# Kernel optimization log

Measured on AMD Instinct MI355X. Metric: run time of the kernel, lower is better.

## Reference

```python
import jax, jax.numpy as jnp
import numpy as np

DIM = 180
HEADS = 6
HEAD_DIM = DIM // HEADS  # 30
WS = 16                  # window size
PWS = WS // 2            # permuted window size (8)
N = WS * WS              # 256 tokens per window
M = PWS * PWS            # 64 pooled kv tokens per window
B = 4                    # batch (images)
NW = 256                 # windows per image
BW = B * NW              # total windows (b_)
SCALE = HEAD_DIM ** -0.5


def _aligned_rel_index():
    # replicates the buffer construction in __init__ (torch.meshgrid default = 'ij')
    coords = np.stack(np.meshgrid(np.arange(PWS), np.arange(PWS), indexing='ij'))
    cf = coords.reshape(2, -1)
    rel = (cf[:, :, None] - cf[:, None, :]).transpose(1, 2, 0).copy()
    rel[:, :, 0] += PWS - 1
    rel[:, :, 1] += PWS - 1
    rel[:, :, 0] *= 2 * PWS - 1
    idx = rel.sum(-1)  # (M, M)
    idx = idx.reshape(PWS, PWS, 1, 1, M)
    idx = np.tile(idx, (1, 1, 2, 2, 1)).transpose(0, 2, 1, 3, 4).reshape(4 * M, M)
    return idx  # (N, M)


def setup_inputs() -> dict:
    key = jax.random.key(0)
    ks = jax.random.split(key, 10)
    num_bias = (2 * PWS - 1) * (2 * PWS - 1)  # 225
    inp = {
        'x': jax.random.normal(ks[0], (BW, N, DIM), jnp.float32),
        'k_v': jax.random.normal(ks[1], (B, 256), jnp.float32),
        'mask': jnp.zeros((NW, N, M), jnp.float32),
        'W_kernel': jax.random.normal(ks[2], (DIM * 2, 256), jnp.float32) * 0.02,
        'W_q': jax.random.normal(ks[3], (DIM, DIM), jnp.float32) * 0.02,
        'b_q': jnp.zeros((DIM,), jnp.float32),
        'W_kv': jax.random.normal(ks[4], (DIM // 2, DIM), jnp.float32) * 0.02,
        'b_kv': jnp.zeros((DIM // 2,), jnp.float32),
        'bias_table': jax.random.normal(ks[5], (num_bias, HEADS), jnp.float32) * 0.02,
        'W_proj': jax.random.normal(ks[6], (DIM, DIM), jnp.float32) * 0.02,
        'b_proj': jnp.zeros((DIM,), jnp.float32),
        'rel_index': jnp.asarray(_aligned_rel_index(), jnp.int32),
        'b': B,
        'windows_size': WS,
    }
    return inp


def reference(x, k_v, mask, W_kernel, W_q, b_q, W_kv, b_kv, bias_table,
              W_proj, b_proj, rel_index, b, windows_size):
    b_, n, c = x.shape
    # FiLM-style modulation: per-image scale/shift broadcast over all windows/tokens
    kv_mod = (k_v @ W_kernel.T).reshape(-1, 1, 1, 1, c * 2)   # (b,1,1,1,2c)
    k_v1, k_v2 = jnp.split(kv_mod, 2, axis=4)
    xr = x.reshape(b, -1, windows_size, windows_size, c)
    x = (xr * k_v1 + k_v2).reshape(b_, n, c)

    # pooled kv: 2x2 spatial pool packed into channels, split into k and v
    kv = (x @ W_kv.T + b_kv)
    kv = kv.reshape(b_, PWS, 2, PWS, 2, 2, c // 4)
    kv = kv.transpose(0, 1, 3, 5, 2, 4, 6).reshape(b_, n // 4, 2, HEADS, c // HEADS)
    kv = kv.transpose(2, 0, 3, 1, 4)                          # (2, b_, h, n//4, d)
    k, v = kv[0], kv[1]

    q = (x @ W_q.T + b_q).reshape(b_, n, HEADS, HEAD_DIM).transpose(0, 2, 1, 3)
    q = q * SCALE                                             # (b_, h, n, d)

    attn = jnp.einsum('bhnd,bhmd->bhnm', q, k)                # (b_, h, n, n//4)

    # gathered relative position bias
    rpb = bias_table[rel_index.reshape(-1)].reshape(n, n // 4, HEADS)
    attn = attn + rpb.transpose(2, 0, 1)[None]

    nw = mask.shape[0]
    attn = attn.reshape(b_ // nw, nw, HEADS, n, n // 4) + mask[None, :, None]
    attn = attn.reshape(-1, HEADS, n, n // 4)
    attn = jax.nn.softmax(attn, axis=-1)

    out = jnp.einsum('bhnm,bhmd->bhnd', attn, v)
    out = out.transpose(0, 2, 1, 3).reshape(b_, n, c)
    return out @ W_proj.T + b_proj
```

## Files before the change

### kernel.cpp

```cpp
#include <hip/hip_runtime.h>
#include <stdint.h>


#define NHEADS 6
#define SCALE_Q 0.18257418583505536f

#define KVM_OFF   0
#define WCAT_OFF  1440
#define WPROJ_OFF 29088
#define BCAT_OFF  47520
#define RPB_OFF   47808
#define BUF_DW    146112

typedef _Float16 half2v __attribute__((ext_vector_type(2)));
typedef _Float16 f16x8  __attribute__((ext_vector_type(8)));
typedef float    f32x4  __attribute__((ext_vector_type(4)));

__device__ __forceinline__ uint32_t pkf16(float lo, float hi) {
    return __builtin_bit_cast(uint32_t, __builtin_amdgcn_cvt_pkrtz(lo, hi));
}
__device__ __forceinline__ unsigned short f16b(float v) {
    return __builtin_bit_cast(unsigned short, (_Float16)v);
}

__global__ __launch_bounds__(256) void prep_kernel(
    const float* __restrict__ k_v, const float* __restrict__ W_kernel,
    const float* __restrict__ W_q, const float* __restrict__ b_q,
    const float* __restrict__ W_kv, const float* __restrict__ b_kv,
    const float* __restrict__ W_proj, const float* __restrict__ bias_table,
    const int* __restrict__ rel_index, float* __restrict__ ws)
{
    const int bid = blockIdx.x, tid = threadIdx.x;
    uint32_t* wsd = (uint32_t*)ws;
    if (bid < 6) {
        const int j = bid * 256 + tid;
        if (j < 1440) {
            const int img = j / 360;
            const int o = j - img * 360;
            const float* kr = k_v + img * 256;
            const float* wr = W_kernel + o * 256;
            float s0 = 0.f, s1 = 0.f, s2 = 0.f, s3 = 0.f;
            for (int t = 0; t < 256; t += 4) {
                s0 = fmaf(kr[t + 0], wr[t + 0], s0);
                s1 = fmaf(kr[t + 1], wr[t + 1], s1);
                s2 = fmaf(kr[t + 2], wr[t + 2], s2);
                s3 = fmaf(kr[t + 3], wr[t + 3], s3);
            }
            ws[KVM_OFF + j] = (s0 + s1) + (s2 + s3);
        }
    } else if (bid < 114) {
        const int i = (bid - 6) * 256 + tid;
        if (i < 27648) {
            const int j = i / 96, k0 = (i - j * 96) * 2;
            float v0 = 0.f, v1 = 0.f;
            if (j < 180) {
                if (k0 < 180)     v0 = W_q[j * 180 + k0] * SCALE_Q;
                if (k0 + 1 < 180) v1 = W_q[j * 180 + k0 + 1] * SCALE_Q;
            } else if (j < 270) {
                const int jj = j - 180;
                if (k0 < 180)     v0 = W_kv[jj * 180 + k0];
                if (k0 + 1 < 180) v1 = W_kv[jj * 180 + k0 + 1];
            }
            wsd[WCAT_OFF + i] = pkf16(v0, v1);
        }
    } else if (bid < 186) {
        const int i = (bid - 114) * 256 + tid;
        if (i < 18432) {
            const int j = i / 96, k0 = (i - j * 96) * 2;
            float v0 = (j < 180 && k0 < 180)     ? W_proj[j * 180 + k0]     : 0.f;
            float v1 = (j < 180 && k0 + 1 < 180) ? W_proj[j * 180 + k0 + 1] : 0.f;
            wsd[WPROJ_OFF + i] = pkf16(v0, v1);
        }
    } else if (bid == 186) {
        if (tid < 288) {
            float b = 0.f;
            if (tid < 180)      b = b_q[tid] * SCALE_Q;
            else if (tid < 270) b = b_kv[tid - 180];
            ws[BCAT_OFF + tid] = b;
        }
    } else {
        const int i = (bid - 187) * 256 + tid;
        if (i < 98304) {
            const int m = i & 63, t = (i >> 6) & 255, h = i >> 14;
            ws[RPB_OFF + i] = bias_table[rel_index[t * 64 + m] * NHEADS + h];
        }
    }
}

__global__ __launch_bounds__(512, 2) void fused_qkv_attn(
    const float* __restrict__ x, const float* __restrict__ mask,
    const float* __restrict__ ws_f, _Float16* __restrict__ buf)
{
    __shared__ __attribute__((aligned(16))) char As[98304];
    __shared__ __attribute__((aligned(16))) char Kls[24576];
    __shared__ __attribute__((aligned(16))) char Vt[24576];

    const int tid = threadIdx.x;
    const int win = blockIdx.x;
    const int img = win >> 8;
    const int w   = win & 255;
    const int lane = tid & 63, wv = tid >> 6;
    const int lr = lane & 15, lk = lane >> 4;
    const int wrow = wv * 32;

    const uint32_t* wsd = (const uint32_t*)ws_f;
    const _Float16* wcat = (const _Float16*)(wsd + WCAT_OFF);
    const float*    kvs  = ws_f + KVM_OFF + img * 360;

    for (int it = 0; it < 12; ++it) {
        const int idx = it * 512 + tid;
        const int r = idx / 24, c = idx - r * 24;
        const float* xr = x + ((size_t)win * 256 + r) * 180;
        const int c0 = c * 8;
        float v[8];
        if (c0 + 8 <= 180) {
            float4 x0 = *(const float4*)(xr + c0);
            float4 x1 = *(const float4*)(xr + c0 + 4);
            v[0] = x0.x; v[1] = x0.y; v[2] = x0.z; v[3] = x0.w;
            v[4] = x1.x; v[5] = x1.y; v[6] = x1.z; v[7] = x1.w;
#pragma unroll
            for (int e = 0; e < 8; ++e)
                v[e] = fmaf(v[e], kvs[c0 + e], kvs[180 + c0 + e]);
        } else {
#pragma unroll
            for (int e = 0; e < 8; ++e) {
                const int cc = c0 + e;
                v[e] = (cc < 180) ? fmaf(xr[cc], kvs[cc], kvs[180 + cc]) : 0.f;
            }
        }
        uint4 pk;
        pk.x = pkf16(v[0], v[1]); pk.y = pkf16(v[2], v[3]);
        pk.z = pkf16(v[4], v[5]); pk.w = pkf16(v[6], v[7]);
        *(uint4*)(As + r * 384 + ((c ^ (r & 7)) << 4)) = pk;
    }
    if (tid < 384) {
        const int h = tid >> 6, mm = tid & 63;
        *(uint32_t*)(Kls + h * 2048 + mm * 64 + ((3 ^ ((mm >> 1) & 3)) << 4) + 12) = 0u;
    }
    __syncthreads();

    const float* bcat = ws_f + BCAT_OFF;

    f32x4 acc1[2][9];
#pragma unroll
    for (int a = 0; a < 2; ++a)
#pragma unroll
        for (int b = 0; b < 9; ++b) acc1[a][b] = (f32x4){0.f, 0.f, 0.f, 0.f};
    for (int kk = 0; kk < 6; ++kk) {
        f16x8 bf[9];
#pragma unroll
        for (int nf = 0; nf < 9; ++nf)
            bf[nf] = *(const f16x8*)(wcat + (size_t)(144 + nf * 16 + lr) * 192 + kk * 32 + lk * 8);
        f16x8 af[2];
#pragma unroll
        for (int mf = 0; mf < 2; ++mf) {
            const int r = wrow + mf * 16 + lr;
            af[mf] = *(const f16x8*)(As + r * 384 + (((kk * 4 + lk) ^ (r & 7)) << 4));
        }
#pragma unroll
        for (int mf = 0; mf < 2; ++mf)
#pragma unroll
            for (int nf = 0; nf < 9; ++nf)
                acc1[mf][nf] = __builtin_amdgcn_mfma_f32_16x16x32_f16(af[mf], bf[nf], acc1[mf][nf], 0, 0, 0);
    }
#pragma unroll
    for (int nf = 0; nf < 9; ++nf) {
        const float bb = bcat[144 + nf * 16 + lr];
#pragma unroll
        for (int mf = 0; mf < 2; ++mf)
#pragma unroll
            for (int rr = 0; rr < 4; ++rr) acc1[mf][nf][rr] += bb;
    }

#pragma unroll
    for (int mf = 0; mf < 2; ++mf)
#pragma unroll
        for (int nf = 2; nf < 8; ++nf)
#pragma unroll
            for (int rr = 0; rr < 4; ++rr) {
                const int j = 144 + nf * 16 + lr - 180;
                if (j >= 0 && j < 90) {
                    const int t = wrow + mf * 16 + lk * 4 + rr;
                    const int i1 = t >> 5, aa = (t >> 4) & 1, i2 = (t >> 1) & 7, a2 = t & 1;
                    const int mm = i1 * 8 + i2;
                    const int base = aa * 90 + a2 * 45;
                    const int d45 = (j < 45) ? j : j - 45;
                    const int flat = base + d45;
                    const int h = (flat * 2185) >> 16;
                    const int d = flat - h * 30;
                    const unsigned short hv = f16b(acc1[mf][nf][rr]);
                    if (j < 45)
                        *(unsigned short*)(Kls + h * 2048 + mm * 64 +
                            ((((unsigned)d >> 3) ^ ((mm >> 1) & 3)) << 4) + (d & 7) * 2) = hv;
                    else
                        *(unsigned short*)(Vt + h * 4096 + d * 128 +
                            ((((unsigned)mm >> 3) ^ (d & 7)) << 4) + (mm & 7) * 2) = hv;
                }
            }

    {
        uint32_t* bufd = (uint32_t*)buf;
#pragma unroll
        for (int z = 0; z < 3; ++z) {
            const int idx = z * 64 + lane;
            const int r = idx / 6, c = idx - r * 6;
            bufd[((size_t)win * 256 + wrow + r) * 96 + 90 + c] = 0u;
        }
    }

    f32x4 acc0[2][9];
#pragma unroll
    for (int a = 0; a < 2; ++a)
#pragma unroll
        for (int b = 0; b < 9; ++b) acc0[a][b] = (f32x4){0.f, 0.f, 0.f, 0.f};
    for (int kk = 0; kk < 6; ++kk) {
        f16x8 bf[9];
#pragma unroll
        for (int nf = 0; nf < 9; ++nf)
            bf[nf] = *(const f16x8*)(wcat + (size_t)(nf * 16 + lr) * 192 + kk * 32 + lk * 8);
        f16x8 af[2];
#pragma unroll
        for (int mf = 0; mf < 2; ++mf) {
            const int r = wrow + mf * 16 + lr;
            af[mf] = *(const f16x8*)(As + r * 384 + (((kk * 4 + lk) ^ (r & 7)) << 4));
        }
#pragma unroll
        for (int mf = 0; mf < 2; ++mf)
#pragma unroll
            for (int nf = 0; nf < 9; ++nf)
                acc0[mf][nf] = __builtin_amdgcn_mfma_f32_16x16x32_f16(af[mf], bf[nf], acc0[mf][nf], 0, 0, 0);
    }
#pragma unroll
    for (int nf = 0; nf < 9; ++nf) {
        const float bb = bcat[nf * 16 + lr];
#pragma unroll
        for (int mf = 0; mf < 2; ++mf)
#pragma unroll
            for (int rr = 0; rr < 4; ++rr) acc0[mf][nf][rr] += bb;
    }
    __syncthreads();

    char* qscW = As + wv * 2048;
    char* PW   = As + 16384 + wv * 4096;
    if (lane < 32)
        *(uint32_t*)(qscW + lane * 64 + ((3 ^ ((lane >> 1) & 3)) << 4) + 12) = 0u;

    const float* rpb0 = ws_f + RPB_OFF;

#pragma unroll
    for (int h = 0; h < NHEADS; ++h) {
#pragma unroll
        for (int pf = 0; pf < 12; ++pf) {
            const int colbase = pf * 16;
            if (colbase + 16 > 30 * h && colbase < 30 * h + 30) {
#pragma unroll
                for (int mf = 0; mf < 2; ++mf)
#pragma unroll
                    for (int rr = 0; rr < 4; ++rr) {
                        const int d = colbase + lr - 30 * h;
                        if (d >= 0 && d < 30) {
                            const float qv = (pf < 9) ? acc0[mf][pf][rr] : acc1[mf][pf - 9][rr];
                            const int rL = mf * 16 + lk * 4 + rr;
                            *(unsigned short*)(qscW + rL * 64 +
                                ((((unsigned)d >> 3) ^ ((rL >> 1) & 3)) << 4) + (d & 7) * 2) = f16b(qv);
                        }
                    }
            }
        }

        f16x8 qf[2], kf[4];
#pragma unroll
        for (int qt = 0; qt < 2; ++qt) {
            const int rL = qt * 16 + lr;
            qf[qt] = *(const f16x8*)(qscW + rL * 64 + ((lk ^ ((rL >> 1) & 3)) << 4));
        }
#pragma unroll
        for (int mt = 0; mt < 4; ++mt) {
            const int mm = mt * 16 + lr;
            kf[mt] = *(const f16x8*)(Kls + h * 2048 + mm * 64 + ((lk ^ ((mm >> 1) & 3)) << 4));
        }
        f32x4 sa[2][4];
        const float* rpb = rpb0 + (h << 14);
#pragma unroll
        for (int qt = 0; qt < 2; ++qt)
#pragma unroll
            for (int mt = 0; mt < 4; ++mt)
#pragma unroll
                for (int rr = 0; rr < 4; ++rr) {
                    const int t = wrow + qt * 16 + lk * 4 + rr;
                    const int m = mt * 16 + lr;
                    sa[qt][mt][rr] = rpb[(t << 6) + m] + mask[(((w << 8) + t) << 6) + m];
                }
#pragma unroll
        for (int qt = 0; qt < 2; ++qt)
#pragma unroll
            for (int mt = 0; mt < 4; ++mt)
                sa[qt][mt] = __builtin_amdgcn_mfma_f32_16x16x32_f16(qf[qt], kf[mt], sa[qt][mt], 0, 0, 0);

        float invv[2][4];
#pragma unroll
        for (int qt = 0; qt < 2; ++qt) {
            float mx[4], sm[4];
#pragma unroll
            for (int rr = 0; rr < 4; ++rr)
                mx[rr] = fmaxf(fmaxf(sa[qt][0][rr], sa[qt][1][rr]),
                               fmaxf(sa[qt][2][rr], sa[qt][3][rr]));
#pragma unroll
            for (int xm = 1; xm < 16; xm <<= 1)
#pragma unroll
                for (int rr = 0; rr < 4; ++rr)
                    mx[rr] = fmaxf(mx[rr], __shfl_xor(mx[rr], xm));
#pragma unroll
            for (int mt = 0; mt < 4; ++mt)
#pragma unroll
                for (int rr = 0; rr < 4; ++rr)
                    sa[qt][mt][rr] = __expf(sa[qt][mt][rr] - mx[rr]);
#pragma unroll
            for (int rr = 0; rr < 4; ++rr)
                sm[rr] = (sa[qt][0][rr] + sa[qt][1][rr]) + (sa[qt][2][rr] + sa[qt][3][rr]);
#pragma unroll
            for (int xm = 1; xm < 16; xm <<= 1)
#pragma unroll
                for (int rr = 0; rr < 4; ++rr)
                    sm[rr] += __shfl_xor(sm[rr], xm);
#pragma unroll
            for (int rr = 0; rr < 4; ++rr) invv[qt][rr] = 1.0f / sm[rr];
#pragma unroll
            for (int mt = 0; mt < 4; ++mt)
#pragma unroll
                for (int rr = 0; rr < 4; ++rr) {
                    const int rL = qt * 16 + lk * 4 + rr;
                    const int m = mt * 16 + lr;
                    *(unsigned short*)(PW + rL * 128 +
                        ((((unsigned)m >> 3) ^ (rL & 7)) << 4) + (m & 7) * 2) = f16b(sa[qt][mt][rr]);
                }
        }

        f32x4 oa[2][2];
#pragma unroll
        for (int a = 0; a < 2; ++a)
#pragma unroll
            for (int b = 0; b < 2; ++b) oa[a][b] = (f32x4){0.f, 0.f, 0.f, 0.f};
#pragma unroll
        for (int ks = 0; ks < 2; ++ks) {
            f16x8 pa[2], vb[2];
#pragma unroll
            for (int qt = 0; qt < 2; ++qt) {
                const int rL = qt * 16 + lr;
                pa[qt] = *(const f16x8*)(PW + rL * 128 + (((ks * 4 + lk) ^ (rL & 7)) << 4));
            }
#pragma unroll
            for (int df = 0; df < 2; ++df) {
                const int d = df * 16 + lr;
                vb[df] = *(const f16x8*)(Vt + h * 4096 + d * 128 + (((ks * 4 + lk) ^ (d & 7)) << 4));
            }
#pragma unroll
            for (int qt = 0; qt < 2; ++qt)
#pragma unroll
                for (int df = 0; df < 2; ++df)
                    oa[qt][df] = __builtin_amdgcn_mfma_f32_16x16x32_f16(pa[qt], vb[df], oa[qt][df], 0, 0, 0);
        }

#pragma unroll
        for (int qt = 0; qt < 2; ++qt)
#pragma unroll
            for (int df = 0; df < 2; ++df)
#pragma unroll
                for (int rr = 0; rr < 4; ++rr) {
                    const int d = df * 16 + lr;
                    if (d < 30) {
                        const float v = oa[qt][df][rr] * invv[qt][rr];
                        const size_t row = (size_t)win * 256 + wrow + qt * 16 + lk * 4 + rr;
                        buf[row * 192 + h * 30 + d] = (_Float16)v;
                    }
                }
    }
}

__global__ __launch_bounds__(256, 3) void proj_gemm(
    const float* __restrict__ ws_f, const _Float16* __restrict__ buf,
    const float* __restrict__ b_proj, float* __restrict__ out)
{
    __shared__ __attribute__((aligned(16))) char As[64 * 384];
    const int tid = threadIdx.x;
    const int m0 = blockIdx.x * 64;
    const _Float16* wproj = (const _Float16*)((const uint32_t*)ws_f + WPROJ_OFF);

    for (int it = 0; it < 6; ++it) {
        const int idx = it * 256 + tid;
        const int r = idx / 24, c = idx - r * 24;
        const uint4 v = *(const uint4*)(buf + (size_t)(m0 + r) * 192 + c * 8);
        *(uint4*)(As + r * 384 + ((c ^ (r & 7)) << 4)) = v;
    }
    __syncthreads();

    const int lane = tid & 63, wid = tid >> 6;
    const int wr0 = (wid & 1) * 32;
    const int wc0 = (wid >> 1) * 96;
    const int lr = lane & 15, lk = lane >> 4;

    f32x4 acc[2][6];
#pragma unroll
    for (int a = 0; a < 2; ++a)
#pragma unroll
        for (int b = 0; b < 6; ++b) acc[a][b] = (f32x4){0.f, 0.f, 0.f, 0.f};

#pragma unroll 2
    for (int kk = 0; kk < 6; ++kk) {
        f16x8 bf[6];
#pragma unroll
        for (int nf = 0; nf < 6; ++nf)
            bf[nf] = *(const f16x8*)(wproj + (size_t)(wc0 + nf * 16 + lr) * 192 + kk * 32 + lk * 8);
        f16x8 af[2];
#pragma unroll
        for (int mf = 0; mf < 2; ++mf) {
            const int r = wr0 + mf * 16 + lr;
            af[mf] = *(const f16x8*)(As + r * 384 + (((kk * 4 + lk) ^ (r & 7)) << 4));
        }
#pragma unroll
        for (int mf = 0; mf < 2; ++mf)
#pragma unroll
            for (int nf = 0; nf < 6; ++nf)
                acc[mf][nf] = __builtin_amdgcn_mfma_f32_16x16x32_f16(af[mf], bf[nf], acc[mf][nf], 0, 0, 0);
    }

#pragma unroll
    for (int mf = 0; mf < 2; ++mf) {
#pragma unroll
        for (int nf = 0; nf < 6; ++nf) {
            const int j = wc0 + nf * 16 + lr;
            if (j < 180) {
                const float bb = b_proj[j];
                const int mr = m0 + wr0 + mf * 16 + lk * 4;
#pragma unroll
                for (int rr = 0; rr < 4; ++rr)
                    out[(size_t)(mr + rr) * 180 + j] = acc[mf][nf][rr] + bb;
            }
        }
    }
}

extern "C" void kernel_launch(void* const* d_in, const int* in_sizes, int n_in,
                              void* d_out, int out_size, void* d_ws, size_t ws_size,
                              hipStream_t stream)
{
    (void)in_sizes; (void)n_in; (void)out_size; (void)ws_size;
    const float* x          = (const float*)d_in[0];
    const float* k_v        = (const float*)d_in[1];
    const float* mask       = (const float*)d_in[2];
    const float* W_kernel   = (const float*)d_in[3];
    const float* W_q        = (const float*)d_in[4];
    const float* b_q        = (const float*)d_in[5];
    const float* W_kv       = (const float*)d_in[6];
    const float* b_kv       = (const float*)d_in[7];
    const float* bias_table = (const float*)d_in[8];
    const float* W_proj     = (const float*)d_in[9];
    const float* b_proj     = (const float*)d_in[10];
    const int*   rel_index  = (const int*)d_in[11];

    float* ws = (float*)d_ws;
    _Float16* buf = (_Float16*)((uint32_t*)d_ws + BUF_DW);

    prep_kernel<<<571, 256, 0, stream>>>(k_v, W_kernel, W_q, b_q, W_kv, b_kv,
                                         W_proj, bias_table, rel_index, ws);
    fused_qkv_attn<<<1024, 512, 0, stream>>>(x, mask, ws, buf);
    proj_gemm<<<4096, 256, 0, stream>>>(ws, buf, b_proj, (float*)d_out);
}
```

Measured before the change: 423.8 us.

## Drop shared x staging, load A fragments directly, and raise attention occupancy

The fused QKV+attention kernel no longer stages the modulated x tile in a 96KB LDS buffer. Each wave now builds its A fragments straight from global memory, applying the FiLM modulation in registers. The Q/KV GEMMs are split into three 96-column passes, with Q kept packed as fp16 in registers, and attention is processed per 16-row q-tile to cut register pressure. LDS falls to about 80KB and launch bounds ask for 4 blocks per CU. The relative-position-bias table is transposed so each lane can read four consecutive query rows as one float4. In exchange, x is re-read from global memory for every column pass, and K heads are spaced 4096 bytes apart.

```diff
diff --git a/kernel.cpp b/kernel.cpp
--- a/kernel.cpp
+++ b/kernel.cpp
@@ -12,15 +12,17 @@
 #define RPB_OFF   47808
 #define BUF_DW    146112
 
-typedef _Float16 half2v __attribute__((ext_vector_type(2)));
-typedef _Float16 f16x8  __attribute__((ext_vector_type(8)));
-typedef float    f32x4  __attribute__((ext_vector_type(4)));
+typedef _Float16 f16x8 __attribute__((ext_vector_type(8)));
+typedef float    f32x4 __attribute__((ext_vector_type(4)));
 
 __device__ __forceinline__ uint32_t pkf16(float lo, float hi) {
     return __builtin_bit_cast(uint32_t, __builtin_amdgcn_cvt_pkrtz(lo, hi));
 }
 __device__ __forceinline__ unsigned short f16b(float v) {
     return __builtin_bit_cast(unsigned short, (_Float16)v);
+}
+__device__ __forceinline__ f32x4 mfma16(f16x8 a, f16x8 b, f32x4 c) {
+    return __builtin_amdgcn_mfma_f32_16x16x32_f16(a, b, c, 0, 0, 0);
 }
 
 __global__ __launch_bounds__(256) void prep_kernel(
@@ -81,19 +83,19 @@
     } else {
         const int i = (bid - 187) * 256 + tid;
         if (i < 98304) {
-            const int m = i & 63, t = (i >> 6) & 255, h = i >> 14;
+            const int t = i & 255, m = (i >> 8) & 63, h = i >> 14;
             ws[RPB_OFF + i] = bias_table[rel_index[t * 64 + m] * NHEADS + h];
         }
     }
 }
 
-__global__ __launch_bounds__(512, 2) void fused_qkv_attn(
+__global__ __launch_bounds__(512, 4) void fused_qkv_attn(
     const float* __restrict__ x, const float* __restrict__ mask,
     const float* __restrict__ ws_f, _Float16* __restrict__ buf)
 {
-    __shared__ __attribute__((aligned(16))) char As[98304];
     __shared__ __attribute__((aligned(16))) char Kls[24576];
     __shared__ __attribute__((aligned(16))) char Vt[24576];
+    __shared__ __attribute__((aligned(16))) char Scr[32768];
 
     const int tid = threadIdx.x;
     const int win = blockIdx.x;
@@ -106,97 +108,128 @@
     const uint32_t* wsd = (const uint32_t*)ws_f;
     const _Float16* wcat = (const _Float16*)(wsd + WCAT_OFF);
     const float*    kvs  = ws_f + KVM_OFF + img * 360;
-
-    for (int it = 0; it < 12; ++it) {
-        const int idx = it * 512 + tid;
-        const int r = idx / 24, c = idx - r * 24;
-        const float* xr = x + ((size_t)win * 256 + r) * 180;
-        const int c0 = c * 8;
-        float v[8];
-        if (c0 + 8 <= 180) {
-            float4 x0 = *(const float4*)(xr + c0);
-            float4 x1 = *(const float4*)(xr + c0 + 4);
-            v[0] = x0.x; v[1] = x0.y; v[2] = x0.z; v[3] = x0.w;
-            v[4] = x1.x; v[5] = x1.y; v[6] = x1.z; v[7] = x1.w;
-#pragma unroll
-            for (int e = 0; e < 8; ++e)
-                v[e] = fmaf(v[e], kvs[c0 + e], kvs[180 + c0 + e]);
-        } else {
-#pragma unroll
-            for (int e = 0; e < 8; ++e) {
-                const int cc = c0 + e;
-                v[e] = (cc < 180) ? fmaf(xr[cc], kvs[cc], kvs[180 + cc]) : 0.f;
-            }
-        }
-        uint4 pk;
-        pk.x = pkf16(v[0], v[1]); pk.y = pkf16(v[2], v[3]);
-        pk.z = pkf16(v[4], v[5]); pk.w = pkf16(v[6], v[7]);
-        *(uint4*)(As + r * 384 + ((c ^ (r & 7)) << 4)) = pk;
-    }
+    const float*    bcat = ws_f + BCAT_OFF;
+
     if (tid < 384) {
         const int h = tid >> 6, mm = tid & 63;
-        *(uint32_t*)(Kls + h * 2048 + mm * 64 + ((3 ^ ((mm >> 1) & 3)) << 4) + 12) = 0u;
-    }
-    __syncthreads();
-
-    const float* bcat = ws_f + BCAT_OFF;
-
-    f32x4 acc1[2][9];
-#pragma unroll
-    for (int a = 0; a < 2; ++a)
-#pragma unroll
-        for (int b = 0; b < 9; ++b) acc1[a][b] = (f32x4){0.f, 0.f, 0.f, 0.f};
-    for (int kk = 0; kk < 6; ++kk) {
-        f16x8 bf[9];
-#pragma unroll
-        for (int nf = 0; nf < 9; ++nf)
-            bf[nf] = *(const f16x8*)(wcat + (size_t)(144 + nf * 16 + lr) * 192 + kk * 32 + lk * 8);
-        f16x8 af[2];
-#pragma unroll
-        for (int mf = 0; mf < 2; ++mf) {
-            const int r = wrow + mf * 16 + lr;
-            af[mf] = *(const f16x8*)(As + r * 384 + (((kk * 4 + lk) ^ (r & 7)) << 4));
-        }
-#pragma unroll
-        for (int mf = 0; mf < 2; ++mf)
-#pragma unroll
-            for (int nf = 0; nf < 9; ++nf)
-                acc1[mf][nf] = __builtin_amdgcn_mfma_f32_16x16x32_f16(af[mf], bf[nf], acc1[mf][nf], 0, 0, 0);
-    }
-#pragma unroll
-    for (int nf = 0; nf < 9; ++nf) {
-        const float bb = bcat[144 + nf * 16 + lr];
-#pragma unroll
-        for (int mf = 0; mf < 2; ++mf)
-#pragma unroll
-            for (int rr = 0; rr < 4; ++rr) acc1[mf][nf][rr] += bb;
-    }
-
-#pragma unroll
-    for (int mf = 0; mf < 2; ++mf)
-#pragma unroll
-        for (int nf = 2; nf < 8; ++nf)
-#pragma unroll
-            for (int rr = 0; rr < 4; ++rr) {
-                const int j = 144 + nf * 16 + lr - 180;
-                if (j >= 0 && j < 90) {
-                    const int t = wrow + mf * 16 + lk * 4 + rr;
-                    const int i1 = t >> 5, aa = (t >> 4) & 1, i2 = (t >> 1) & 7, a2 = t & 1;
-                    const int mm = i1 * 8 + i2;
-                    const int base = aa * 90 + a2 * 45;
-                    const int d45 = (j < 45) ? j : j - 45;
-                    const int flat = base + d45;
-                    const int h = (flat * 2185) >> 16;
-                    const int d = flat - h * 30;
-                    const unsigned short hv = f16b(acc1[mf][nf][rr]);
-                    if (j < 45)
-                        *(unsigned short*)(Kls + h * 2048 + mm * 64 +
-                            ((((unsigned)d >> 3) ^ ((mm >> 1) & 3)) << 4) + (d & 7) * 2) = hv;
-                    else
-                        *(unsigned short*)(Vt + h * 4096 + d * 128 +
-                            ((((unsigned)mm >> 3) ^ (d & 7)) << 4) + (mm & 7) * 2) = hv;
-                }
-            }
+        *(uint32_t*)(Kls + h * 4096 + mm * 64 + ((3u ^ ((mm >> 1) & 3)) << 4) + 12) = 0u;
+    }
+
+    const float* xr0 = x + ((size_t)win * 256 + wrow + lr) * 180;
+    const float* xr1 = xr0 + 16 * 180;
+
+    auto load_af = [&](const float* xrow, int c0) -> f16x8 {
+        union { uint32_t u[4]; f16x8 v; } cv;
+        if (c0 + 8 <= 180) {
+            float4 a  = *(const float4*)(xrow + c0);
+            float4 b  = *(const float4*)(xrow + c0 + 4);
+            float4 s0 = *(const float4*)(kvs + c0);
+            float4 s1 = *(const float4*)(kvs + c0 + 4);
+            float4 h0 = *(const float4*)(kvs + 180 + c0);
+            float4 h1 = *(const float4*)(kvs + 180 + c0 + 4);
+            cv.u[0] = pkf16(fmaf(a.x, s0.x, h0.x), fmaf(a.y, s0.y, h0.y));
+            cv.u[1] = pkf16(fmaf(a.z, s0.z, h0.z), fmaf(a.w, s0.w, h0.w));
+            cv.u[2] = pkf16(fmaf(b.x, s1.x, h1.x), fmaf(b.y, s1.y, h1.y));
+            cv.u[3] = pkf16(fmaf(b.z, s1.z, h1.z), fmaf(b.w, s1.w, h1.w));
+        } else if (c0 < 180) {
+            float4 a  = *(const float4*)(xrow + 176);
+            float4 s0 = *(const float4*)(kvs + 176);
+            float4 h0 = *(const float4*)(kvs + 356);
+            cv.u[0] = pkf16(fmaf(a.x, s0.x, h0.x), fmaf(a.y, s0.y, h0.y));
+            cv.u[1] = pkf16(fmaf(a.z, s0.z, h0.z), fmaf(a.w, s0.w, h0.w));
+            cv.u[2] = 0u; cv.u[3] = 0u;
+        } else {
+            cv.u[0] = cv.u[1] = cv.u[2] = cv.u[3] = 0u;
+        }
+        return cv.v;
+    };
+
+    auto run6 = [&](int cb, f32x4 (&acc)[2][6]) {
+#pragma unroll
+        for (int kk = 0; kk < 6; ++kk) {
+            const int c0 = kk * 32 + lk * 8;
+            f16x8 a0 = load_af(xr0, c0);
+            f16x8 a1 = load_af(xr1, c0);
+#pragma unroll
+            for (int nf = 0; nf < 6; ++nf) {
+                f16x8 bf = *(const f16x8*)(wcat + (size_t)(cb + nf * 16 + lr) * 192 + c0);
+                acc[0][nf] = mfma16(a0, bf, acc[0][nf]);
+                acc[1][nf] = mfma16(a1, bf, acc[1][nf]);
+            }
+        }
+    };
+
+    {
+        f32x4 akv[2][6];
+#pragma unroll
+        for (int a = 0; a < 2; ++a)
+#pragma unroll
+            for (int b = 0; b < 6; ++b) akv[a][b] = (f32x4){0.f, 0.f, 0.f, 0.f};
+        run6(176, akv);
+#pragma unroll
+        for (int nf = 0; nf < 6; ++nf) {
+            const int col = 176 + nf * 16 + lr;
+            const int j = col - 180;
+            if (j >= 0 && j < 90) {
+                const float bb = bcat[col];
+                const int d45 = (j < 45) ? j : j - 45;
+#pragma unroll
+                for (int mf = 0; mf < 2; ++mf)
+#pragma unroll
+                    for (int rr = 0; rr < 4; ++rr) {
+                        const int t = wrow + mf * 16 + lk * 4 + rr;
+                        const int mm = ((t >> 5) << 3) + ((t >> 1) & 7);
+                        const int base = ((t >> 4) & 1) * 90 + (t & 1) * 45;
+                        const int flat = base + d45;
+                        const int h = (flat * 2185) >> 16;
+                        const int d = flat - h * 30;
+                        const unsigned short hv = f16b(akv[mf][nf][rr] + bb);
+                        if (j < 45)
+                            *(unsigned short*)(Kls + h * 4096 + mm * 64 +
+                                ((((unsigned)d >> 3) ^ ((mm >> 1) & 3)) << 4) + (d & 7) * 2) = hv;
+                        else
+                            *(unsigned short*)(Vt + h * 4096 + d * 128 +
+                                ((((unsigned)mm >> 3) ^ (d & 7)) << 4) + (mm & 7) * 2) = hv;
+                    }
+            }
+        }
+    }
+
+    uint32_t qp[2][12][2];
+    {
+        f32x4 aq[2][6];
+#pragma unroll
+        for (int a = 0; a < 2; ++a)
+#pragma unroll
+            for (int b = 0; b < 6; ++b) aq[a][b] = (f32x4){0.f, 0.f, 0.f, 0.f};
+        run6(0, aq);
+#pragma unroll
+        for (int nf = 0; nf < 6; ++nf) {
+            const float bb = bcat[nf * 16 + lr];
+#pragma unroll
+            for (int mf = 0; mf < 2; ++mf) {
+                qp[mf][nf][0] = pkf16(aq[mf][nf][0] + bb, aq[mf][nf][1] + bb);
+                qp[mf][nf][1] = pkf16(aq[mf][nf][2] + bb, aq[mf][nf][3] + bb);
+            }
+        }
+    }
+    {
+        f32x4 aq[2][6];
+#pragma unroll
+        for (int a = 0; a < 2; ++a)
+#pragma unroll
+            for (int b = 0; b < 6; ++b) aq[a][b] = (f32x4){0.f, 0.f, 0.f, 0.f};
+        run6(96, aq);
+#pragma unroll
+        for (int nf = 0; nf < 6; ++nf) {
+            const float bb = bcat[96 + nf * 16 + lr];
+#pragma unroll
+            for (int mf = 0; mf < 2; ++mf) {
+                qp[mf][6 + nf][0] = pkf16(aq[mf][nf][0] + bb, aq[mf][nf][1] + bb);
+                qp[mf][6 + nf][1] = pkf16(aq[mf][nf][2] + bb, aq[mf][nf][3] + bb);
+            }
+        }
+    }
 
     {
         uint32_t* bufd = (uint32_t*)buf;
@@ -208,103 +241,68 @@
         }
     }
 
-    f32x4 acc0[2][9];
-#pragma unroll
-    for (int a = 0; a < 2; ++a)
-#pragma unroll
-        for (int b = 0; b < 9; ++b) acc0[a][b] = (f32x4){0.f, 0.f, 0.f, 0.f};
-    for (int kk = 0; kk < 6; ++kk) {
-        f16x8 bf[9];
-#pragma unroll
-        for (int nf = 0; nf < 9; ++nf)
-            bf[nf] = *(const f16x8*)(wcat + (size_t)(nf * 16 + lr) * 192 + kk * 32 + lk * 8);
-        f16x8 af[2];
-#pragma unroll
-        for (int mf = 0; mf < 2; ++mf) {
-            const int r = wrow + mf * 16 + lr;
-            af[mf] = *(const f16x8*)(As + r * 384 + (((kk * 4 + lk) ^ (r & 7)) << 4));
-        }
-#pragma unroll
-        for (int mf = 0; mf < 2; ++mf)
-#pragma unroll
-            for (int nf = 0; nf < 9; ++nf)
-                acc0[mf][nf] = __builtin_amdgcn_mfma_f32_16x16x32_f16(af[mf], bf[nf], acc0[mf][nf], 0, 0, 0);
-    }
-#pragma unroll
-    for (int nf = 0; nf < 9; ++nf) {
-        const float bb = bcat[nf * 16 + lr];
-#pragma unroll
-        for (int mf = 0; mf < 2; ++mf)
-#pragma unroll
-            for (int rr = 0; rr < 4; ++rr) acc0[mf][nf][rr] += bb;
-    }
     __syncthreads();
 
-    char* qscW = As + wv * 2048;
-    char* PW   = As + 16384 + wv * 4096;
+    char* scr = Scr + wv * 4096;
+    char* Pw  = scr + 2048;
+    const float* rpbt = ws_f + RPB_OFF;
+
     if (lane < 32)
-        *(uint32_t*)(qscW + lane * 64 + ((3 ^ ((lane >> 1) & 3)) << 4) + 12) = 0u;
-
-    const float* rpb0 = ws_f + RPB_OFF;
+        *(uint32_t*)(scr + lane * 64 + ((3u ^ ((lane >> 1) & 3)) << 4) + 12) = 0u;
 
 #pragma unroll
     for (int h = 0; h < NHEADS; ++h) {
 #pragma unroll
-        for (int pf = 0; pf < 12; ++pf) {
-            const int colbase = pf * 16;
-            if (colbase + 16 > 30 * h && colbase < 30 * h + 30) {
-#pragma unroll
-                for (int mf = 0; mf < 2; ++mf)
-#pragma unroll
-                    for (int rr = 0; rr < 4; ++rr) {
-                        const int d = colbase + lr - 30 * h;
-                        if (d >= 0 && d < 30) {
-                            const float qv = (pf < 9) ? acc0[mf][pf][rr] : acc1[mf][pf - 9][rr];
-                            const int rL = mf * 16 + lk * 4 + rr;
-                            *(unsigned short*)(qscW + rL * 64 +
-                                ((((unsigned)d >> 3) ^ ((rL >> 1) & 3)) << 4) + (d & 7) * 2) = f16b(qv);
+        for (int nf = 0; nf < 12; ++nf) {
+            if (nf * 16 + 15 >= 30 * h && nf * 16 < 30 * h + 30) {
+                const int d = nf * 16 + lr - 30 * h;
+                if (d >= 0 && d < 30) {
+#pragma unroll
+                    for (int mf = 0; mf < 2; ++mf)
+#pragma unroll
+                        for (int rp = 0; rp < 2; ++rp) {
+                            const int rL = mf * 16 + lk * 4 + rp * 2;
+                            char* p0 = scr + rL * 64 +
+                                ((((unsigned)d >> 3) ^ ((rL >> 1) & 3)) << 4) + (d & 7) * 2;
+                            const uint32_t q2 = qp[mf][nf][rp];
+                            *(unsigned short*)p0        = (unsigned short)(q2 & 0xffffu);
+                            *(unsigned short*)(p0 + 64) = (unsigned short)(q2 >> 16);
                         }
-                    }
-            }
-        }
-
-        f16x8 qf[2], kf[4];
+                }
+            }
+        }
+
 #pragma unroll
         for (int qt = 0; qt < 2; ++qt) {
-            const int rL = qt * 16 + lr;
-            qf[qt] = *(const f16x8*)(qscW + rL * 64 + ((lk ^ ((rL >> 1) & 3)) << 4));
-        }
-#pragma unroll
-        for (int mt = 0; mt < 4; ++mt) {
-            const int mm = mt * 16 + lr;
-            kf[mt] = *(const f16x8*)(Kls + h * 2048 + mm * 64 + ((lk ^ ((mm >> 1) & 3)) << 4));
-        }
-        f32x4 sa[2][4];
-        const float* rpb = rpb0 + (h << 14);
-#pragma unroll
-        for (int qt = 0; qt < 2; ++qt)
-#pragma unroll
-            for (int mt = 0; mt < 4; ++mt)
-#pragma unroll
-                for (int rr = 0; rr < 4; ++rr) {
-                    const int t = wrow + qt * 16 + lk * 4 + rr;
-                    const int m = mt * 16 + lr;
-                    sa[qt][mt][rr] = rpb[(t << 6) + m] + mask[(((w << 8) + t) << 6) + m];
-                }
-#pragma unroll
-        for (int qt = 0; qt < 2; ++qt)
-#pragma unroll
-            for (int mt = 0; mt < 4; ++mt)
-                sa[qt][mt] = __builtin_amdgcn_mfma_f32_16x16x32_f16(qf[qt], kf[mt], sa[qt][mt], 0, 0, 0);
-
-        float invv[2][4];
-#pragma unroll
-        for (int qt = 0; qt < 2; ++qt) {
-            float mx[4], sm[4];
+            const int rq = qt * 16 + lr;
+            f16x8 qf = *(const f16x8*)(scr + rq * 64 +
+                (((unsigned)lk ^ ((rq >> 1) & 3)) << 4));
+
+            f32x4 sa[4];
+            const int t0 = wrow + qt * 16 + lk * 4;
+#pragma unroll
+            for (int mt = 0; mt < 4; ++mt) {
+                const int m = mt * 16 + lr;
+                const float4 rv = *(const float4*)(rpbt + (((size_t)(h * 64 + m)) << 8) + t0);
+                const float* mk = mask + ((((size_t)w << 8) + t0) << 6) + m;
+                sa[mt][0] = rv.x + mk[0];
+                sa[mt][1] = rv.y + mk[64];
+                sa[mt][2] = rv.z + mk[128];
+                sa[mt][3] = rv.w + mk[192];
+            }
+
+#pragma unroll
+            for (int mt = 0; mt < 4; ++mt) {
+                const int mm = mt * 16 + lr;
+                f16x8 kf = *(const f16x8*)(Kls + h * 4096 + mm * 64 +
+                    (((unsigned)lk ^ ((mm >> 1) & 3)) << 4));
+                sa[mt] = mfma16(qf, kf, sa[mt]);
+            }
+
+            float mx[4], sm[4], inv[4];
 #pragma unroll
             for (int rr = 0; rr < 4; ++rr)
-                mx[rr] = fmaxf(fmaxf(sa[qt][0][rr], sa[qt][1][rr]),
-                               fmaxf(sa[qt][2][rr], sa[qt][3][rr]));
+                mx[rr] = fmaxf(fmaxf(sa[0][rr], sa[1][rr]), fmaxf(sa[2][rr], sa[3][rr]));
 #pragma unroll
             for (int xm = 1; xm < 16; xm <<= 1)
 #pragma unroll
@@ -314,66 +312,56 @@
             for (int mt = 0; mt < 4; ++mt)
 #pragma unroll
                 for (int rr = 0; rr < 4; ++rr)
-                    sa[qt][mt][rr] = __expf(sa[qt][mt][rr] - mx[rr]);
+                    sa[mt][rr] = __expf(sa[mt][rr] - mx[rr]);
 #pragma unroll
             for (int rr = 0; rr < 4; ++rr)
-                sm[rr] = (sa[qt][0][rr] + sa[qt][1][rr]) + (sa[qt][2][rr] + sa[qt][3][rr]);
+                sm[rr] = (sa[0][rr] + sa[1][rr]) + (sa[2][rr] + sa[3][rr]);
 #pragma unroll
             for (int xm = 1; xm < 16; xm <<= 1)
 #pragma unroll
                 for (int rr = 0; rr < 4; ++rr)
                     sm[rr] += __shfl_xor(sm[rr], xm);
 #pragma unroll
-            for (int rr = 0; rr < 4; ++rr) invv[qt][rr] = 1.0f / sm[rr];
-#pragma unroll
-            for (int mt = 0; mt < 4; ++mt)
+            for (int rr = 0; rr < 4; ++rr) inv[rr] = 1.0f / sm[rr];
+
+#pragma unroll
+            for (int mt = 0; mt < 4; ++mt) {
+                const int m = mt * 16 + lr;
 #pragma unroll
                 for (int rr = 0; rr < 4; ++rr) {
-                    const int rL = qt * 16 + lk * 4 + rr;
-                    const int m = mt * 16 + lr;
-                    *(unsigned short*)(PW + rL * 128 +
-                        ((((unsigned)m >> 3) ^ (rL & 7)) << 4) + (m & 7) * 2) = f16b(sa[qt][mt][rr]);
+                    const int r16 = lk * 4 + rr;
+                    *(unsigned short*)(Pw + r16 * 128 +
+                        ((((unsigned)m >> 3) ^ (r16 & 7)) << 4) + (m & 7) * 2) = f16b(sa[mt][rr]);
                 }
-        }
-
-        f32x4 oa[2][2];
-#pragma unroll
-        for (int a = 0; a < 2; ++a)
-#pragma unroll
-            for (int b = 0; b < 2; ++b) oa[a][b] = (f32x4){0.f, 0.f, 0.f, 0.f};
-#pragma unroll
-        for (int ks = 0; ks < 2; ++ks) {
-            f16x8 pa[2], vb[2];
-#pragma unroll
-            for (int qt = 0; qt < 2; ++qt) {
-                const int rL = qt * 16 + lr;
-                pa[qt] = *(const f16x8*)(PW + rL * 128 + (((ks * 4 + lk) ^ (rL & 7)) << 4));
-            }
+            }
+
+            f32x4 oa[2];
+            oa[0] = (f32x4){0.f, 0.f, 0.f, 0.f};
+            oa[1] = (f32x4){0.f, 0.f, 0.f, 0.f};
+#pragma unroll
+            for (int ks = 0; ks < 2; ++ks) {
+                f16x8 pa = *(const f16x8*)(Pw + lr * 128 +
+                    ((((unsigned)(ks * 4 + lk)) ^ (lr & 7)) << 4));
+#pragma unroll
+                for (int df = 0; df < 2; ++df) {
+                    const int d = df * 16 + lr;
+                    f16x8 vb = *(const f16x8*)(Vt + h * 4096 + d * 128 +
+                        ((((unsigned)(ks * 4 + lk)) ^ (d & 7)) << 4));
+                    oa[df] = mfma16(pa, vb, oa[df]);
+                }
+            }
+
+            const size_t rowb = (size_t)win * 256 + wrow + qt * 16 + lk * 4;
 #pragma unroll
             for (int df = 0; df < 2; ++df) {
                 const int d = df * 16 + lr;
-                vb[df] = *(const f16x8*)(Vt + h * 4096 + d * 128 + (((ks * 4 + lk) ^ (d & 7)) << 4));
-            }
-#pragma unroll
-            for (int qt = 0; qt < 2; ++qt)
-#pragma unroll
-                for (int df = 0; df < 2; ++df)
-                    oa[qt][df] = __builtin_amdgcn_mfma_f32_16x16x32_f16(pa[qt], vb[df], oa[qt][df], 0, 0, 0);
-        }
-
-#pragma unroll
-        for (int qt = 0; qt < 2; ++qt)
-#pragma unroll
-            for (int df = 0; df < 2; ++df)
-#pragma unroll
-                for (int rr = 0; rr < 4; ++rr) {
-                    const int d = df * 16 + lr;
-                    if (d < 30) {
-                        const float v = oa[qt][df][rr] * invv[qt][rr];
-                        const size_t row = (size_t)win * 256 + wrow + qt * 16 + lk * 4 + rr;
-                        buf[row * 192 + h * 30 + d] = (_Float16)v;
-                    }
+                if (d < 30) {
+#pragma unroll
+                    for (int rr = 0; rr < 4; ++rr)
+                        buf[(rowb + rr) * 192 + h * 30 + d] = (_Float16)(oa[df][rr] * inv[rr]);
                 }
+            }
+        }
     }
 }
 
@@ -421,7 +409,7 @@
         for (int mf = 0; mf < 2; ++mf)
 #pragma unroll
             for (int nf = 0; nf < 6; ++nf)
-                acc[mf][nf] = __builtin_amdgcn_mfma_f32_16x16x32_f16(af[mf], bf[nf], acc[mf][nf], 0, 0, 0);
+                acc[mf][nf] = mfma16(af[mf], bf[nf], acc[mf][nf]);
     }
 
 #pragma unroll
```

After: 532.9 us. 25.7% more time.
